# Kernel optimization log

Hardware: AMD Instinct MI355X
Metric: run time of the kernel (lower is better)

The kernel has to match this reference:

```python
import jax, jax.numpy as jnp
import numpy as np

B, T = 4096, 512          # batch, max seq len
V, E, H, O = 57, 20, 128, 18  # vocab, embed, hidden, classes


def setup_inputs() -> dict:
    key = jax.random.key(0)
    ks = jax.random.split(key, 9)
    x = jax.random.randint(ks[0], (B, T), 0, V)
    lens = jax.random.randint(ks[1], (B,), 1, T + 1)
    x_lengths = jnp.sort(lens)[::-1]  # pack_padded_sequence needs descending lengths
    s = 1.0 / np.sqrt(H)
    emb = jax.random.normal(ks[2], (V, E), dtype=jnp.float32)
    W_ih = jax.random.uniform(ks[3], (H, E), minval=-s, maxval=s, dtype=jnp.float32)
    W_hh = jax.random.uniform(ks[4], (H, H), minval=-s, maxval=s, dtype=jnp.float32)
    b_ih = jax.random.uniform(ks[5], (H,), minval=-s, maxval=s, dtype=jnp.float32)
    b_hh = jax.random.uniform(ks[6], (H,), minval=-s, maxval=s, dtype=jnp.float32)
    so = 1.0 / np.sqrt(H)
    W_out = jax.random.uniform(ks[7], (O, H), minval=-so, maxval=so, dtype=jnp.float32)
    b_out = jax.random.uniform(ks[8], (O,), minval=-so, maxval=so, dtype=jnp.float32)
    return {"x": x, "x_lengths": x_lengths, "emb": emb, "W_ih": W_ih,
            "W_hh": W_hh, "b_ih": b_ih, "b_hh": b_hh, "W_out": W_out, "b_out": b_out}


def reference(x, x_lengths, emb, W_ih, W_hh, b_ih, b_hh, W_out, b_out):
    xe = emb[x]                                            # [B,T,E] embedding gather
    # precompute input projection + both biases once (hoisted out of recurrence)
    xw = jnp.einsum('bte,he->bth', xe, W_ih) + b_ih + b_hh  # [B,T,H]
    valid = jnp.arange(T)[None, :] < x_lengths[:, None]     # [B,T] packed-seq mask

    def step(h, inp):
        xw_t, v_t = inp                                     # [B,H], [B]
        h_new = jnp.tanh(xw_t + h @ W_hh.T)
        # packed RNN: stop updating once past this sequence's length,
        # so the final h equals the hidden state at step len-1
        h = jnp.where(v_t[:, None], h_new, h)
        return h, None

    h0 = jnp.zeros((B, H), dtype=xw.dtype)
    hT, _ = jax.lax.scan(step, h0, (jnp.swapaxes(xw, 0, 1), valid.T))  # scan over T
    logits = jax.nn.relu(hT) @ W_out.T + b_out              # [B,O]
    return jax.nn.log_softmax(logits, axis=1)
```

## Files before the change

kernel.cpp:

```cpp
#include <hip/hip_runtime.h>
#include <math.h>

#define Bn 4096
#define Tn 512
#define Vn 57
#define En 20
#define Hn 128
#define On 18
#define ROWS 16
#define NTHR 512
#define NBLK (Bn / ROWS)
#define XWSTR 132
#define XBSTR 516
#define HFSTR 132
#define ASCALE 2.8853900817779268f

typedef _Float16 half8  __attribute__((ext_vector_type(8)));
typedef __fp16   fp16x2 __attribute__((ext_vector_type(2)));
typedef float    floatx4 __attribute__((ext_vector_type(4)));

__device__ __forceinline__ float tanh_scaled(float z) {
    float e = __builtin_amdgcn_exp2f(z);
    float r = __builtin_amdgcn_rcpf(e + 1.0f);
    return fmaf(-2.0f, r, 1.0f);
}

__device__ __forceinline__ unsigned pk_u32(fp16x2 v) {
    union { fp16x2 h; unsigned u; } c; c.h = v; return c.u;
}

__launch_bounds__(NTHR, 2)
__global__ void rnn_mfma_kernel(const int* __restrict__ x,
                                const int* __restrict__ xlen,
                                const float* __restrict__ emb,
                                const float* __restrict__ W_ih,
                                const float* __restrict__ W_hh,
                                const float* __restrict__ b_ih,
                                const float* __restrict__ b_hh,
                                const float* __restrict__ W_out,
                                const float* __restrict__ b_out,
                                float* __restrict__ out)
{
    __shared__ __align__(16) uint4 exB[2][4][64];
    __shared__ unsigned sCtr;
    __shared__ __align__(16) float sXW[Vn * XWSTR];
    __shared__ __align__(16) float sHf[ROWS * HFSTR];
    __shared__ __align__(16) unsigned char sXb[ROWS * XBSTR];
    __shared__ float sLogit[ROWS][On];
    __shared__ float sMLS[ROWS];
    __shared__ float sPad[6200];

    const int tid  = threadIdx.x;
    const int blk  = blockIdx.x;
    const int row0 = blk * ROWS;

    ((volatile float*)sPad)[tid % 6200] = 0.0f;

    const int w    = tid >> 6;
    const int lane = tid & 63;
    const int n    = lane & 15;
    const int q    = lane >> 4;
    const int kcW  = w >> 1;
    const int bsel = w & 1;

    half8 Ah[4];
    const int f = 32 * kcW + 8 * (n >> 2) + 4 * bsel + (n & 3);
    #pragma unroll
    for (int kc = 0; kc < 4; ++kc) {
        const float* p = &W_hh[f * Hn + kc * 32 + q * 8];
        #pragma unroll
        for (int i = 0; i < 8; ++i)
            Ah[kc][i] = (_Float16)(p[i] * ASCALE);
    }

    for (int idx = tid; idx < Vn * Hn; idx += NTHR) {
        int vo = idx >> 7, ff = idx & 127;
        float acc = b_ih[ff] + b_hh[ff];
        #pragma unroll
        for (int e = 0; e < En; ++e)
            acc = fmaf(emb[vo * En + e], W_ih[ff * En + e], acc);
        sXW[vo * XWSTR + ff] = acc * ASCALE;
    }
    for (int idx = tid * 4; idx < ROWS * Tn; idx += NTHR * 4) {
        int4 v = *(const int4*)&x[row0 * Tn + idx];
        int r = idx >> 9, t = idx & 511;
        uchar4 bb;
        bb.x = (unsigned char)v.x; bb.y = (unsigned char)v.y;
        bb.z = (unsigned char)v.z; bb.w = (unsigned char)v.w;
        *(uchar4*)&sXb[r * XBSTR + t] = bb;
    }
    for (int idx = tid; idx < 2 * 4 * 64; idx += NTHR)
        ((uint4*)exB)[idx] = make_uint4(0u, 0u, 0u, 0u);
    if (tid == 0) sCtr = 0u;
    __syncthreads();

    const int Lmax  = xlen[row0];
    const int len_n = xlen[row0 + n];
    const int wOffH = 32 * kcW + 8 * q + 4 * bsel;

    int    idN;
    float4 XWc;
    {
        int id0 = sXb[n * XBSTR];
        XWc = *(const float4*)&sXW[id0 * XWSTR + wOffH];
        idN = sXb[n * XBSTR + (Lmax > 1 ? 1 : 0)];
    }
    float hreg[4] = {0.f, 0.f, 0.f, 0.f};

    #define RNN_STEP(BR, BW, t)                                                   \
    {                                                                             \
        float4 XWn = *(const float4*)&sXW[idN * XWSTR + wOffH];                   \
        int tn = (t) + 2;                                                         \
        int idN2 = sXb[n * XBSTR + (tn < Lmax ? tn : Lmax - 1)];                  \
        const unsigned tgt = 8u * (unsigned)(t);                                  \
        int spin = 0;                                                             \
        while (((volatile unsigned*)&sCtr)[0] < tgt) {                            \
            if (++spin > (1 << 20)) break;                                        \
        }                                                                         \
        __asm__ __volatile__("" ::: "memory");                                    \
        half8 bf0 = *(const half8*)&exB[BR][0][lane];                             \
        half8 bf1 = *(const half8*)&exB[BR][1][lane];                             \
        half8 bf2 = *(const half8*)&exB[BR][2][lane];                             \
        half8 bf3 = *(const half8*)&exB[BR][3][lane];                             \
        floatx4 aE = {XWc.x, XWc.y, XWc.z, XWc.w};                                \
        floatx4 aO = {0.f, 0.f, 0.f, 0.f};                                        \
        aE = __builtin_amdgcn_mfma_f32_16x16x32_f16(Ah[0], bf0, aE, 0, 0, 0);     \
        aO = __builtin_amdgcn_mfma_f32_16x16x32_f16(Ah[1], bf1, aO, 0, 0, 0);     \
        aE = __builtin_amdgcn_mfma_f32_16x16x32_f16(Ah[2], bf2, aE, 0, 0, 0);     \
        aO = __builtin_amdgcn_mfma_f32_16x16x32_f16(Ah[3], bf3, aO, 0, 0, 0);     \
        const bool upd = ((t) < len_n);                                           \
        _Pragma("unroll")                                                         \
        for (int i = 0; i < 4; ++i) {                                             \
            float v = tanh_scaled(aE[i] + aO[i]);                                 \
            hreg[i] = upd ? v : hreg[i];                                          \
        }                                                                         \
        uint2 pk;                                                                 \
        pk.x = pk_u32(__builtin_amdgcn_cvt_pkrtz(hreg[0], hreg[1]));              \
        pk.y = pk_u32(__builtin_amdgcn_cvt_pkrtz(hreg[2], hreg[3]));              \
        *(uint2*)((_Float16*)&exB[BW][kcW][0] + lane * 8 + 4 * bsel) = pk;        \
        __asm__ __volatile__("s_waitcnt lgkmcnt(0)" ::: "memory");                \
        if (lane == 0) atomicAdd(&sCtr, 1u);                                      \
        XWc = XWn; idN = idN2;                                                    \
    }

    int t = 0;
    for (; t + 2 <= Lmax; t += 2) {
        RNN_STEP(0, 1, t);
        RNN_STEP(1, 0, t + 1);
    }
    if (t < Lmax) {
        RNN_STEP(0, 1, t);
    }
    #undef RNN_STEP

    {
        float4 f0;
        f0.x = hreg[0]; f0.y = hreg[1]; f0.z = hreg[2]; f0.w = hreg[3];
        *(float4*)&sHf[n * HFSTR + wOffH] = f0;
    }
    __syncthreads();

    for (int it = tid; it < ROWS * On; it += NTHR) {
        int r = it / On, c = it % On;
        float acc = b_out[c];
        for (int k = 0; k < Hn; ++k) {
            float hv = sHf[r * HFSTR + k];
            hv = hv > 0.0f ? hv : 0.0f;
            acc = fmaf(hv, W_out[c * Hn + k], acc);
        }
        sLogit[r][c] = acc;
    }
    __syncthreads();

    if (tid < ROWS) {
        float m = -INFINITY;
        #pragma unroll
        for (int c = 0; c < On; ++c) m = fmaxf(m, sLogit[tid][c]);
        float s = 0.0f;
        #pragma unroll
        for (int c = 0; c < On; ++c) s += __expf(sLogit[tid][c] - m);
        sMLS[tid] = m + __logf(s);
    }
    __syncthreads();

    for (int it = tid; it < ROWS * On; it += NTHR) {
        int r = it / On, c = it % On;
        out[(row0 + r) * On + c] = sLogit[r][c] - sMLS[r];
    }
}

extern "C" void kernel_launch(void* const* d_in, const int* in_sizes, int n_in,
                              void* d_out, int out_size, void* d_ws, size_t ws_size,
                              hipStream_t stream) {
    const int*   x     = (const int*)d_in[0];
    const int*   xlen  = (const int*)d_in[1];
    const float* emb   = (const float*)d_in[2];
    const float* W_ih  = (const float*)d_in[3];
    const float* W_hh  = (const float*)d_in[4];
    const float* b_ih  = (const float*)d_in[5];
    const float* b_hh  = (const float*)d_in[6];
    const float* W_out = (const float*)d_in[7];
    const float* b_out = (const float*)d_in[8];
    float*       out   = (float*)d_out;

    rnn_mfma_kernel<<<NBLK, NTHR, 0, stream>>>(x, xlen, emb, W_ih, W_hh,
                                               b_ih, b_hh, W_out, b_out, out);
}
```

Before: 273.7 us.

## Replace atomic counter barrier with epoch-tagged hidden-state exchange in LDS

Drops the shared atomic step counter and its spin-wait. Each wave now embeds an epoch tag in an unused high exponent bit of the packed fp16 hidden values it writes to the LDS exchange buffer. Readers poll the buffer until every tag matches the expected epoch, then mask the tag bits off before the MFMAs. This removes the per-step lgkmcnt wait and atomic on the recurrence's critical path. It relies on 64-bit LDS stores being seen whole and on |h| staying below 2 so the tag bit is free.

```diff
diff --git a/kernel.cpp b/kernel.cpp
--- a/kernel.cpp
+++ b/kernel.cpp
@@ -14,6 +14,7 @@
 #define XBSTR 516
 #define HFSTR 132
 #define ASCALE 2.8853900817779268f
+#define TAGM  0x40000000u
 
 typedef _Float16 half8  __attribute__((ext_vector_type(8)));
 typedef __fp16   fp16x2 __attribute__((ext_vector_type(2)));
@@ -27,6 +28,10 @@
 
 __device__ __forceinline__ unsigned pk_u32(fp16x2 v) {
     union { fp16x2 h; unsigned u; } c; c.h = v; return c.u;
+}
+
+__device__ __forceinline__ half8 as_half8(uint4 v) {
+    union { uint4 u; half8 h; } c; c.u = v; return c.h;
 }
 
 __launch_bounds__(NTHR, 2)
@@ -42,7 +47,6 @@
                                 float* __restrict__ out)
 {
     __shared__ __align__(16) uint4 exB[2][4][64];
-    __shared__ unsigned sCtr;
     __shared__ __align__(16) float sXW[Vn * XWSTR];
     __shared__ __align__(16) float sHf[ROWS * HFSTR];
     __shared__ __align__(16) unsigned char sXb[ROWS * XBSTR];
@@ -89,9 +93,11 @@
         bb.z = (unsigned char)v.z; bb.w = (unsigned char)v.w;
         *(uchar4*)&sXb[r * XBSTR + t] = bb;
     }
-    for (int idx = tid; idx < 2 * 4 * 64; idx += NTHR)
-        ((uint4*)exB)[idx] = make_uint4(0u, 0u, 0u, 0u);
-    if (tid == 0) sCtr = 0u;
+    for (int idx = tid; idx < 2 * 4 * 64; idx += NTHR) {
+        uint4 z = make_uint4(0u, 0u, 0u, 0u);
+        if (idx >= 4 * 64) { z.y = TAGM; z.w = TAGM; }
+        ((uint4*)exB)[idx] = z;
+    }
     __syncthreads();
 
     const int Lmax  = xlen[row0];
@@ -107,21 +113,28 @@
     }
     float hreg[4] = {0.f, 0.f, 0.f, 0.f};
 
-    #define RNN_STEP(BR, BW, t)                                                   \
+    #define RNN_STEP(BR, BW, t, RT, WT)                                           \
     {                                                                             \
         float4 XWn = *(const float4*)&sXW[idN * XWSTR + wOffH];                   \
         int tn = (t) + 2;                                                         \
         int idN2 = sXb[n * XBSTR + (tn < Lmax ? tn : Lmax - 1)];                  \
-        const unsigned tgt = 8u * (unsigned)(t);                                  \
-        int spin = 0;                                                             \
-        while (((volatile unsigned*)&sCtr)[0] < tgt) {                            \
-            if (++spin > (1 << 20)) break;                                        \
+        const unsigned et = (RT) << 30;                                           \
+        uint4 u0, u1, u2, u3;                                                     \
+        for (;;) {                                                                \
+            __asm__ __volatile__("" ::: "memory");                                \
+            u0 = exB[BR][0][lane];                                                \
+            u1 = exB[BR][1][lane];                                                \
+            u2 = exB[BR][2][lane];                                                \
+            u3 = exB[BR][3][lane];                                                \
+            unsigned stale = ((u0.y ^ et) | (u0.w ^ et) | (u1.y ^ et) |           \
+                              (u1.w ^ et) | (u2.y ^ et) | (u2.w ^ et) |           \
+                              (u3.y ^ et) | (u3.w ^ et)) & TAGM;                  \
+            if (!__any((int)stale)) break;                                        \
         }                                                                         \
-        __asm__ __volatile__("" ::: "memory");                                    \
-        half8 bf0 = *(const half8*)&exB[BR][0][lane];                             \
-        half8 bf1 = *(const half8*)&exB[BR][1][lane];                             \
-        half8 bf2 = *(const half8*)&exB[BR][2][lane];                             \
-        half8 bf3 = *(const half8*)&exB[BR][3][lane];                             \
+        u0.y &= ~TAGM; u0.w &= ~TAGM; u1.y &= ~TAGM; u1.w &= ~TAGM;               \
+        u2.y &= ~TAGM; u2.w &= ~TAGM; u3.y &= ~TAGM; u3.w &= ~TAGM;               \
+        half8 bf0 = as_half8(u0), bf1 = as_half8(u1);                             \
+        half8 bf2 = as_half8(u2), bf3 = as_half8(u3);                             \
         floatx4 aE = {XWc.x, XWc.y, XWc.z, XWc.w};                                \
         floatx4 aO = {0.f, 0.f, 0.f, 0.f};                                        \
         aE = __builtin_amdgcn_mfma_f32_16x16x32_f16(Ah[0], bf0, aE, 0, 0, 0);     \
@@ -136,20 +149,21 @@
         }                                                                         \
         uint2 pk;                                                                 \
         pk.x = pk_u32(__builtin_amdgcn_cvt_pkrtz(hreg[0], hreg[1]));              \
-        pk.y = pk_u32(__builtin_amdgcn_cvt_pkrtz(hreg[2], hreg[3]));              \
+        pk.y = pk_u32(__builtin_amdgcn_cvt_pkrtz(hreg[2], hreg[3]))               \
+               | ((WT) << 30);                                                    \
         *(uint2*)((_Float16*)&exB[BW][kcW][0] + lane * 8 + 4 * bsel) = pk;        \
-        __asm__ __volatile__("s_waitcnt lgkmcnt(0)" ::: "memory");                \
-        if (lane == 0) atomicAdd(&sCtr, 1u);                                      \
         XWc = XWn; idN = idN2;                                                    \
     }
 
+    unsigned e = 0u;
     int t = 0;
     for (; t + 2 <= Lmax; t += 2) {
-        RNN_STEP(0, 1, t);
-        RNN_STEP(1, 0, t + 1);
+        RNN_STEP(0, 1, t,     e, e);
+        RNN_STEP(1, 0, t + 1, e, e ^ 1u);
+        e ^= 1u;
     }
     if (t < Lmax) {
-        RNN_STEP(0, 1, t);
+        RNN_STEP(0, 1, t, e, e);
     }
     #undef RNN_STEP
 
```

After: 451.1 us. 64.8% more time.
